# Kernel optimization log

Measured on AMD Instinct MI355X. Metric: run time of the kernel, lower is better.

The kernel has to match this reference:

```python
import jax, jax.numpy as jnp
import numpy as np

D = 8        # input_path_dim
S = 64       # cde_state_dim
H = 128      # vf_hidden_dim
OUT = 8      # output_path_dim
T = 2049     # time samples
B = 32       # batch (vmapped)
WIN = 16     # signature_window_size
NWIN = (T - 1) // WIN   # 128 scan steps
II, JJ = np.triu_indices(D, 1)    # Lyndon words of length 2: pairs i<j (P=28)


def setup_inputs() -> dict:
    key = jax.random.key(0)
    ks = jax.random.split(key, 16)
    g = lambda k, shp, fan: (jax.random.normal(k, shp, dtype=jnp.float32) / np.sqrt(fan)).astype(jnp.float32)
    z = lambda n: jnp.zeros((n,), jnp.float32)
    return {
        "ts": jnp.arange(T, dtype=jnp.float32),
        "x": jax.random.normal(ks[0], (B, T, D), dtype=jnp.float32) * 0.1,
        # initial MLP: d -> H -> H -> S, softplus activations
        "Wi0": g(ks[1], (H, D), D), "bi0": z(H),
        "Wi1": g(ks[2], (H, H), H), "bi1": z(H),
        "Wi2": g(ks[3], (S, H), H), "bi2": z(S),
        # vector-field MLP: S -> H -> H -> D*S, softplus hidden, tanh final
        "Wv0": g(ks[4], (H, S), S), "bv0": z(H),
        "Wv1": g(ks[5], (H, H), H), "bv1": z(H),
        "Wv2": g(ks[6], (D * S, H), H), "bv2": z(D * S),
        # readout: S -> OUT
        "Wr": g(ks[7], (OUT, S), S), "br": z(OUT),
    }


def _logsignatures(x):
    """Depth-2 log-signatures of a piecewise-linear path over windows.
    x: (B, T, D). Returns s1: (B, NWIN, D) increments, s2: (B, NWIN, P) Levy areas
    in the Lyndon basis [e_i, e_j], i<j."""
    delta = x[:, 1:] - x[:, :-1]                      # (B, T-1, D)
    delta = delta[:, : NWIN * WIN].reshape(x.shape[0], NWIN, WIN, D)
    s1 = delta.sum(axis=2)                            # (B, NWIN, D)
    cum = jnp.cumsum(delta, axis=2) - delta           # exclusive prefix sums
    M = jnp.einsum("bnwi,bnwj->bnij", cum, delta)    # (B, NWIN, D, D)
    L = 0.5 * (M - jnp.swapaxes(M, -1, -2))           # antisymmetric Levy area
    s2 = L[..., II, JJ]                               # (B, NWIN, P)
    return s1, s2


def reference(ts, x, Wi0, bi0, Wi1, bi1, Wi2, bi2, Wv0, bv0, Wv1, bv1, Wv2, bv2, Wr, br):
    sp = jax.nn.softplus

    def initial(x0):  # (D,) -> (S,)
        z = sp(Wi0 @ x0 + bi0)
        z = sp(Wi1 @ z + bi1)
        return Wi2 @ z + bi2

    def vf(h):  # (S,) -> (D, S): one vector field per input channel
        z = sp(Wv0 @ h + bv0)
        z = sp(Wv1 @ z + bv1)
        return jnp.tanh(Wv2 @ z + bv2).reshape(D, S)

    s1, s2 = _logsignatures(x)

    def single(x0_s, s1_s, s2_s):
        h0 = initial(x0_s)

        def step(h, sig):
            a, b = sig  # depth-1 (D,), depth-2 Lyndon coeffs (P,)
            V = vf(h)                          # (D, S)
            J = jax.jacfwd(vf)(h)              # (D, S, S) Jacobians dV_i/dh
            JV = jnp.einsum("dab,eb->dea", J, V)   # JV[j,i] = J_j @ V_i
            brack = JV[JJ, II] - JV[II, JJ]        # (P, S): [V_i, V_j], i<j
            hn = h + a @ V + b @ brack             # log-ODE step
            return hn, hn

        _, hist = jax.lax.scan(step, h0, (s1_s, s2_s))
        return jnp.concatenate([h0[None], hist], axis=0)   # (NWIN+1, S)

    hist = jax.vmap(single)(x[:, 0], s1, s2)    # (B, NWIN+1, S)
    return jnp.einsum("bns,os->bno", hist, Wr) + br   # evolving readout, identity act
```

## Files before the change

kernel.cpp:

```cpp
#include <hip/hip_runtime.h>
#include <hip/hip_bf16.h>

#define DD 8
#define SS 64
#define HH 128
#define OUTD 8
#define TT 2049
#define BB 32
#define WINW 16
#define NWIN 128
#define PP 28
#define VSTR 516

typedef __attribute__((ext_vector_type(8))) short short8v;
typedef __attribute__((ext_vector_type(4))) float f32x4;

__device__ __forceinline__ float softplus_f(float x){
    return fmaxf(x, 0.f) + __logf(1.f + __expf(-fabsf(x)));
}
__device__ __forceinline__ float tanh_f(float x){
    float e = __expf(2.f * x);
    return 1.f - 2.f / (e + 1.f);
}
__device__ __forceinline__ void sp_sig(float x, float& sp, float& sg){
    float t = __expf(-fabsf(x));
    float r = 1.f / (1.f + t);
    sg = x > 0.f ? r : 1.f - r;
    sp = fmaxf(x, 0.f) - __logf(r);
}
__device__ __forceinline__ unsigned short f2bf(float f){
    return __builtin_bit_cast(unsigned short, __float2bfloat16(f));
}
__device__ __forceinline__ unsigned pk2(float a, float b){
    unsigned lo = (unsigned)__builtin_bit_cast(unsigned short, __float2bfloat16(a));
    unsigned hi = (unsigned)__builtin_bit_cast(unsigned short, __float2bfloat16(b));
    return lo | (hi << 16);
}

__global__ void sig_kernel(const float* __restrict__ x,
                           float* __restrict__ s1o, float* __restrict__ s2o){
    int w = blockIdx.x * blockDim.x + threadIdx.x;
    if (w >= BB * NWIN) return;
    int b = w >> 7, n = w & (NWIN - 1);
    const float* xp = x + ((size_t)b * TT + (size_t)n * WINW) * DD;
    float prev[DD], cum[DD], s1v[DD], M[DD][DD];
    #pragma unroll
    for (int i = 0; i < DD; ++i){
        cum[i] = 0.f; s1v[i] = 0.f;
        #pragma unroll
        for (int j = 0; j < DD; ++j) M[i][j] = 0.f;
    }
    #pragma unroll
    for (int i = 0; i < DD; ++i) prev[i] = xp[i];
    for (int t = 0; t < WINW; ++t){
        float cur[DD], del[DD];
        #pragma unroll
        for (int i = 0; i < DD; ++i) cur[i] = xp[(t + 1) * DD + i];
        #pragma unroll
        for (int i = 0; i < DD; ++i) del[i] = cur[i] - prev[i];
        #pragma unroll
        for (int i = 0; i < DD; ++i){
            #pragma unroll
            for (int j = 0; j < DD; ++j) M[i][j] += cum[i] * del[j];
        }
        #pragma unroll
        for (int i = 0; i < DD; ++i){ cum[i] += del[i]; s1v[i] += del[i]; prev[i] = cur[i]; }
    }
    #pragma unroll
    for (int i = 0; i < DD; ++i) s1o[(size_t)w * DD + i] = s1v[i];
    int p = 0;
    #pragma unroll
    for (int i = 0; i < DD; ++i){
        #pragma unroll
        for (int j = i + 1; j < DD; ++j){ s2o[(size_t)w * PP + p] = 0.5f * (M[i][j] - M[j][i]); ++p; }
    }
}

#define BPOS(k, nn) ((((k) >> 5) * 64 + (((k) >> 3) & 3) * 16 + (nn)) * 8 + ((k) & 7))

__global__ __launch_bounds__(512, 2) void scan_kernel(
    const float* __restrict__ x,
    const float* __restrict__ Wi0, const float* __restrict__ bi0,
    const float* __restrict__ Wi1, const float* __restrict__ bi1,
    const float* __restrict__ Wi2, const float* __restrict__ bi2,
    const float* __restrict__ Wv0, const float* __restrict__ bv0,
    const float* __restrict__ Wv1, const float* __restrict__ bv1,
    const float* __restrict__ Wv2, const float* __restrict__ bv2,
    const float* __restrict__ Wr,  const float* __restrict__ br,
    const float* __restrict__ s1g, const float* __restrict__ s2g,
    float* __restrict__ out)
{
    const int tid = threadIdx.x;
    const int w   = tid >> 6;
    const int l   = tid & 63;
    const int lg  = l >> 4;
    const int ln  = l & 15;
    const int b0  = blockIdx.x * 4;

    __shared__ __align__(16) short BpH[2 * 64 * 8];
    __shared__ __align__(16) short Bp0[4 * 64 * 8];
    __shared__ __align__(16) short Bp1[4 * 64 * 8];
    __shared__ __align__(16) short Bp7[2][2 * 64 * 8];
    __shared__ __align__(16) short Bp8[2][4 * 64 * 8];
    __shared__ __align__(16) short Bp9[2][4 * 64 * 8];
    __shared__ __align__(16) float s0p[4][HH], s1p[4][HH];
    __shared__ __align__(16) float Vl[4 * VSTR], Rf[4 * VSTR];
    __shared__ __align__(16) float hfb[4][2][SS];
    __shared__ __align__(16) float bv0L[HH], bv1L[HH], bv2L[512];
    __shared__ __align__(16) float WrL[OUTD * SS];
    __shared__ float brL[OUTD];
    __shared__ __align__(16) float sAll[4][NWIN * DD];
    __shared__ __align__(16) float bAll[4][NWIN * PP];
    __shared__ __align__(16) float outC[4][32][OUTD];
    __shared__ __align__(16) float Cexp[4][DD][12];

    short8v a0f[2], a1f[4];
    short8v a2f0[4], a2f1[4], a2f2[4], a2f3[4];
    #pragma unroll
    for (int ks = 0; ks < 2; ++ks){
        const float* p = Wv0 + (size_t)(w * 16 + ln) * SS + ks * 32 + lg * 8;
        short8v f;
        #pragma unroll
        for (int j = 0; j < 8; ++j) f[j] = (short)f2bf(p[j]);
        a0f[ks] = f;
    }
    #pragma unroll
    for (int ks = 0; ks < 4; ++ks){
        const float* p = Wv1 + (size_t)(w * 16 + ln) * HH + ks * 32 + lg * 8;
        short8v f;
        #pragma unroll
        for (int j = 0; j < 8; ++j) f[j] = (short)f2bf(p[j]);
        a1f[ks] = f;
    }
    #pragma unroll
    for (int ks = 0; ks < 4; ++ks){
        const float* p0 = Wv2 + (size_t)(64 * w + 0 * 16 + ln) * HH + ks * 32 + lg * 8;
        const float* p1 = Wv2 + (size_t)(64 * w + 1 * 16 + ln) * HH + ks * 32 + lg * 8;
        const float* p2 = Wv2 + (size_t)(64 * w + 2 * 16 + ln) * HH + ks * 32 + lg * 8;
        const float* p3 = Wv2 + (size_t)(64 * w + 3 * 16 + ln) * HH + ks * 32 + lg * 8;
        short8v f0, f1, f2, f3;
        #pragma unroll
        for (int j = 0; j < 8; ++j){
            f0[j] = (short)f2bf(p0[j]); f1[j] = (short)f2bf(p1[j]);
            f2[j] = (short)f2bf(p2[j]); f3[j] = (short)f2bf(p3[j]);
        }
        a2f0[ks] = f0; a2f1[ks] = f1; a2f2[ks] = f2; a2f3[ks] = f3;
    }
    if (tid < HH){ bv0L[tid] = bv0[tid]; bv1L[tid] = bv1[tid]; }
    bv2L[tid] = bv2[tid];
    WrL[tid]  = Wr[tid];
    if (tid < OUTD) brL[tid] = br[tid];
    {
        float* sF = &sAll[0][0];
        for (int i = tid; i < 4 * NWIN * DD; i += 512){
            int c = i >> 10;
            sF[i] = s1g[(size_t)(b0 + c) * (NWIN * DD) + (i & 1023)];
        }
        float* bF = &bAll[0][0];
        for (int i = tid; i < 4 * NWIN * PP; i += 512){
            int c = i / (NWIN * PP);
            bF[i] = s2g[(size_t)(b0 + c) * (NWIN * PP) + (i - c * (NWIN * PP))];
        }
        for (int i = tid; i < 2 * 64 * 8; i += 512) BpH[i] = 0;
        for (int i = tid; i < 4 * 64 * 8; i += 512){ Bp0[i] = 0; Bp1[i] = 0; }
    }
    __syncthreads();

    {
        int c4 = tid >> 7, r = tid & 127;
        float acc = bi0[r];
        const float* x0 = x + (size_t)(b0 + c4) * TT * DD;
        #pragma unroll
        for (int k = 0; k < DD; ++k) acc += Wi0[r * DD + k] * x0[k];
        s0p[c4][r] = softplus_f(acc);
    }
    if (tid < 256){
        int cc = tid >> 6, dd = (tid >> 3) & 7, ee = tid & 7;
        const float* bco = &bAll[cc][0];
        float cv = 0.f;
        if (ee < dd)      cv =  bco[((ee * (15 - ee)) >> 1) + dd - ee - 1];
        else if (ee > dd) cv = -bco[((dd * (15 - dd)) >> 1) + ee - dd - 1];
        Cexp[cc][dd][ee] = cv;
    }
    __syncthreads();
    {
        int c4 = tid >> 7, r = tid & 127;
        float acc = bi1[r];
        const f32x4* wv = (const f32x4*)(Wi1 + (size_t)r * HH);
        const f32x4* zv = (const f32x4*)&s0p[c4][0];
        #pragma unroll 8
        for (int k = 0; k < 32; ++k){
            f32x4 a = wv[k], z = zv[k];
            acc += a.x * z.x + a.y * z.y + a.z * z.z + a.w * z.w;
        }
        s1p[c4][r] = softplus_f(acc);
    }
    __syncthreads();
    if (tid < 256){
        int c4 = tid >> 6, s = tid & 63;
        float acc = bi2[s];
        const f32x4* wv = (const f32x4*)(Wi2 + (size_t)s * HH);
        const f32x4* zv = (const f32x4*)&s1p[c4][0];
        #pragma unroll 8
        for (int k = 0; k < 32; ++k){
            f32x4 a = wv[k], z = zv[k];
            acc += a.x * z.x + a.y * z.y + a.z * z.z + a.w * z.w;
        }
        hfb[c4][0][s] = acc;
        BpH[BPOS(s, c4)] = (short)f2bf(acc);
    }
    __syncthreads();

    const f32x4 zero4 = {0.f, 0.f, 0.f, 0.f};
    const int rb = w * 16 + lg * 4;

    for (int n = 0; n < NWIN; ++n){
        {
            f32x4 acc = zero4;
            acc = __builtin_amdgcn_mfma_f32_16x16x32_bf16(a0f[0], *(const short8v*)&BpH[(0 * 64 + l) * 8], acc, 0, 0, 0);
            acc = __builtin_amdgcn_mfma_f32_16x16x32_bf16(a0f[1], *(const short8v*)&BpH[(1 * 64 + l) * 8], acc, 0, 0, 0);
            if (ln < 4){
                int c = ln;
                f32x4 bv = *(const f32x4*)&bv0L[rb];
                float z[4], sgv[4];
                #pragma unroll
                for (int r = 0; r < 4; ++r){
                    float zz, gg;
                    sp_sig(acc[r] + bv[r], zz, gg);
                    z[r] = zz; sgv[r] = gg;
                }
                f32x4 sg = {sgv[0], sgv[1], sgv[2], sgv[3]};
                *(f32x4*)&s0p[c][rb] = sg;
                uint2 pk; pk.x = pk2(z[0], z[1]); pk.y = pk2(z[2], z[3]);
                *(uint2*)&Bp0[BPOS(rb, c)] = pk;
            }
        }
        __syncthreads();

        {
            f32x4 acc = zero4;
            #pragma unroll
            for (int ks = 0; ks < 4; ++ks)
                acc = __builtin_amdgcn_mfma_f32_16x16x32_bf16(a1f[ks], *(const short8v*)&Bp0[(ks * 64 + l) * 8], acc, 0, 0, 0);
            if (ln < 4){
                int c = ln;
                f32x4 bv = *(const f32x4*)&bv1L[rb];
                float z[4], sgv[4];
                #pragma unroll
                for (int r = 0; r < 4; ++r){
                    float zz, gg;
                    sp_sig(acc[r] + bv[r], zz, gg);
                    z[r] = zz; sgv[r] = gg;
                }
                f32x4 sg = {sgv[0], sgv[1], sgv[2], sgv[3]};
                *(f32x4*)&s1p[c][rb] = sg;
                uint2 pk; pk.x = pk2(z[0], z[1]); pk.y = pk2(z[2], z[3]);
                #pragma unroll
                for (int cc = 0; cc < 4; ++cc) *(uint2*)&Bp1[BPOS(rb, c * 4 + cc)] = pk;
            }
        }
        __syncthreads();

        {
            short8v bf[4];
            #pragma unroll
            for (int ks = 0; ks < 4; ++ks) bf[ks] = *(const short8v*)&Bp1[(ks * 64 + l) * 8];
            f32x4 acc0 = zero4, acc1 = zero4, acc2 = zero4, acc3 = zero4;
            #pragma unroll
            for (int ks = 0; ks < 4; ++ks){
                acc0 = __builtin_amdgcn_mfma_f32_16x16x32_bf16(a2f0[ks], bf[ks], acc0, 0, 0, 0);
                acc1 = __builtin_amdgcn_mfma_f32_16x16x32_bf16(a2f1[ks], bf[ks], acc1, 0, 0, 0);
                acc2 = __builtin_amdgcn_mfma_f32_16x16x32_bf16(a2f2[ks], bf[ks], acc2, 0, 0, 0);
                acc3 = __builtin_amdgcn_mfma_f32_16x16x32_bf16(a2f3[ks], bf[ks], acc3, 0, 0, 0);
            }
            {
                int c = ln >> 2, t = ln & 3;
                f32x4 av = (t == 0) ? acc0 : (t == 1) ? acc1 : (t == 2) ? acc2 : acc3;
                int r4 = 64 * w + t * 16 + lg * 4;
                f32x4 bv = *(const f32x4*)&bv2L[r4];
                f32x4 vv;
                #pragma unroll
                for (int r = 0; r < 4; ++r) vv[r] = tanh_f(av[r] + bv[r]);
                *(f32x4*)&Vl[c * VSTR + r4] = vv;
            }
        }
        __syncthreads();

        {
            int c = tid >> 7, d = (tid >> 4) & 7, s0v = (tid & 15) * 4;
            f32x4 cm0 = *(const f32x4*)&Cexp[c][d][0];
            f32x4 cm1 = *(const f32x4*)&Cexp[c][d][4];
            f32x4 acc = zero4;
            #pragma unroll
            for (int e = 0; e < 8; ++e){
                float ce = (e < 4) ? cm0[e] : cm1[e - 4];
                f32x4 v4 = *(const f32x4*)&Vl[c * VSTR + e * 64 + s0v];
                acc.x += ce * v4.x; acc.y += ce * v4.y;
                acc.z += ce * v4.z; acc.w += ce * v4.w;
            }
            uint2 pk; pk.x = pk2(acc.x, acc.y); pk.y = pk2(acc.z, acc.w);
            *(uint2*)&Bp7[c >> 1][BPOS(s0v, (c & 1) * 8 + d)] = pk;
        }
        __syncthreads();

        {
            #pragma unroll
            for (int p = 0; p < 2; ++p){
                f32x4 acc = zero4;
                acc = __builtin_amdgcn_mfma_f32_16x16x32_bf16(a0f[0], *(const short8v*)&Bp7[p][(0 * 64 + l) * 8], acc, 0, 0, 0);
                acc = __builtin_amdgcn_mfma_f32_16x16x32_bf16(a0f[1], *(const short8v*)&Bp7[p][(1 * 64 + l) * 8], acc, 0, 0, 0);
                int c = 2 * p + (ln >> 3);
                f32x4 sg = *(const f32x4*)&s0p[c][rb];
                uint2 pk; pk.x = pk2(sg[0] * acc[0], sg[1] * acc[1]);
                pk.y = pk2(sg[2] * acc[2], sg[3] * acc[3]);
                *(uint2*)&Bp8[p][BPOS(rb, ln)] = pk;
            }
        }
        __syncthreads();

        {
            #pragma unroll
            for (int p = 0; p < 2; ++p){
                f32x4 acc = zero4;
                #pragma unroll
                for (int ks = 0; ks < 4; ++ks)
                    acc = __builtin_amdgcn_mfma_f32_16x16x32_bf16(a1f[ks], *(const short8v*)&Bp8[p][(ks * 64 + l) * 8], acc, 0, 0, 0);
                int c = 2 * p + (ln >> 3), d = ln & 7;
                f32x4 sg = *(const f32x4*)&s1p[c][rb];
                uint2 pk; pk.x = pk2(sg[0] * acc[0], sg[1] * acc[1]);
                pk.y = pk2(sg[2] * acc[2], sg[3] * acc[3]);
                *(uint2*)&Bp9[d >> 2][BPOS(rb, (d & 3) * 4 + c)] = pk;
            }
        }
        __syncthreads();

        {
            const int im = w >> 2;
            short8v bf[4];
            #pragma unroll
            for (int ks = 0; ks < 4; ++ks) bf[ks] = *(const short8v*)&Bp9[im][(ks * 64 + l) * 8];
            f32x4 acc0 = zero4, acc1 = zero4, acc2 = zero4, acc3 = zero4;
            #pragma unroll
            for (int ks = 0; ks < 4; ++ks){
                acc0 = __builtin_amdgcn_mfma_f32_16x16x32_bf16(a2f0[ks], bf[ks], acc0, 0, 0, 0);
                acc1 = __builtin_amdgcn_mfma_f32_16x16x32_bf16(a2f1[ks], bf[ks], acc1, 0, 0, 0);
                acc2 = __builtin_amdgcn_mfma_f32_16x16x32_bf16(a2f2[ks], bf[ks], acc2, 0, 0, 0);
                acc3 = __builtin_amdgcn_mfma_f32_16x16x32_bf16(a2f3[ks], bf[ks], acc3, 0, 0, 0);
            }
            if ((ln >> 2) == (w & 3)){
                int c = ln & 3;
                #pragma unroll
                for (int t = 0; t < 4; ++t){
                    f32x4 av = (t == 0) ? acc0 : (t == 1) ? acc1 : (t == 2) ? acc2 : acc3;
                    int r4 = 64 * w + t * 16 + lg * 4;
                    f32x4 vv = *(const f32x4*)&Vl[c * VSTR + r4];
                    f32x4 rr;
                    #pragma unroll
                    for (int r = 0; r < 4; ++r) rr[r] = (1.f - vv[r] * vv[r]) * av[r];
                    *(f32x4*)&Rf[c * VSTR + r4] = rr;
                }
            }
        }
        __syncthreads();

        {
            const int cur = n & 1;
            if (w < 4){
                int c = w, s = l;
                f32x4 a0 = *(const f32x4*)&sAll[c][n * DD];
                f32x4 a1 = *(const f32x4*)&sAll[c][n * DD + 4];
                float hN = hfb[c][cur][s];
                #pragma unroll
                for (int d = 0; d < 4; ++d)
                    hN += a0[d] * Vl[c * VSTR + d * 64 + s] + Rf[c * VSTR + d * 64 + s];
                #pragma unroll
                for (int d = 4; d < 8; ++d)
                    hN += a1[d - 4] * Vl[c * VSTR + d * 64 + s] + Rf[c * VSTR + d * 64 + s];
                hfb[c][cur ^ 1][s] = hN;
                BpH[BPOS(s, c)] = (short)f2bf(hN);
            } else {
                {
                    int idx = (w - 4) * 64 + l;
                    int cc = idx >> 6, dd = (idx >> 3) & 7, ee = idx & 7;
                    int nn = (n + 1 < NWIN) ? n + 1 : NWIN - 1;
                    const float* bco = &bAll[cc][nn * PP];
                    float cv = 0.f;
                    if (ee < dd)      cv =  bco[((ee * (15 - ee)) >> 1) + dd - ee - 1];
                    else if (ee > dd) cv = -bco[((dd * (15 - dd)) >> 1) + ee - dd - 1];
                    Cexp[cc][dd][ee] = cv;
                }
                int c = w - 4;
                int o = l >> 3, qq = l & 7;
                f32x4 w0 = *(const f32x4*)&WrL[o * SS + qq * 8];
                f32x4 w1 = *(const f32x4*)&WrL[o * SS + qq * 8 + 4];
                f32x4 h0 = *(const f32x4*)&hfb[c][cur][qq * 8];
                f32x4 h1 = *(const f32x4*)&hfb[c][cur][qq * 8 + 4];
                float acc = w0.x*h0.x + w0.y*h0.y + w0.z*h0.z + w0.w*h0.w
                          + w1.x*h1.x + w1.y*h1.y + w1.z*h1.z + w1.w*h1.w;
                acc += __shfl_xor(acc, 1); acc += __shfl_xor(acc, 2); acc += __shfl_xor(acc, 4);
                if (qq == 0) outC[c][n & 31][o] = brL[o] + acc;
                if ((n & 31) == 31){
                    size_t base = (size_t)(b0 + c) * (NWIN + 1) * OUTD + (size_t)(n - 31) * OUTD;
                    const f32x4* oc = (const f32x4*)&outC[c][0][0];
                    f32x4 v = oc[l];
                    *(f32x4*)&out[base + l * 4] = v;
                }
            }
        }
        __syncthreads();
    }

    if (w >= 4){
        int c = w - 4;
        int o = l >> 3, qq = l & 7;
        f32x4 w0 = *(const f32x4*)&WrL[o * SS + qq * 8];
        f32x4 w1 = *(const f32x4*)&WrL[o * SS + qq * 8 + 4];
        f32x4 h0 = *(const f32x4*)&hfb[c][0][qq * 8];
        f32x4 h1 = *(const f32x4*)&hfb[c][0][qq * 8 + 4];
        float acc = w0.x*h0.x + w0.y*h0.y + w0.z*h0.z + w0.w*h0.w
                  + w1.x*h1.x + w1.y*h1.y + w1.z*h1.z + w1.w*h1.w;
        acc += __shfl_xor(acc, 1); acc += __shfl_xor(acc, 2); acc += __shfl_xor(acc, 4);
        if (qq == 0)
            out[(size_t)(b0 + c) * (NWIN + 1) * OUTD + (size_t)NWIN * OUTD + o] = brL[o] + acc;
    }
}

extern "C" void kernel_launch(void* const* d_in, const int* in_sizes, int n_in,
                              void* d_out, int out_size, void* d_ws, size_t ws_size,
                              hipStream_t stream){
    const float* x   = (const float*)d_in[1];
    const float* Wi0 = (const float*)d_in[2];
    const float* bi0 = (const float*)d_in[3];
    const float* Wi1 = (const float*)d_in[4];
    const float* bi1 = (const float*)d_in[5];
    const float* Wi2 = (const float*)d_in[6];
    const float* bi2 = (const float*)d_in[7];
    const float* Wv0 = (const float*)d_in[8];
    const float* bv0 = (const float*)d_in[9];
    const float* Wv1 = (const float*)d_in[10];
    const float* bv1 = (const float*)d_in[11];
    const float* Wv2 = (const float*)d_in[12];
    const float* bv2 = (const float*)d_in[13];
    const float* Wr  = (const float*)d_in[14];
    const float* br  = (const float*)d_in[15];
    float* out = (float*)d_out;

    float* s1w = (float*)d_ws;
    float* s2w = s1w + (size_t)BB * NWIN * DD;

    sig_kernel<<<(BB * NWIN + 255) / 256, 256, 0, stream>>>(x, s1w, s2w);
    scan_kernel<<<BB / 4, 512, 0, stream>>>(x, Wi0, bi0, Wi1, bi1, Wi2, bi2,
                                            Wv0, bv0, Wv1, bv1, Wv2, bv2,
                                            Wr, br, s1w, s2w, out);
}
```

Baseline: 520.0 us.

## Double scan block to 1024 threads and split MFMA work across 16 waves

Launches the recurrent scan kernel with 1024 threads (16 waves) instead of 512. Each wave now holds half as many Wv2 output rows, and the two Jacobian-vector passes are split across wave halves instead of looped. MFMA accumulation chains are split into two independent accumulators that are summed, which shortens dependency latency. The Cexp precompute moves to otherwise idle waves. The aim is to cut per-step latency on the serial 128-step recurrence, at the cost of more threads taking part in each block barrier.

```diff
diff --git a/kernel.cpp b/kernel.cpp
--- a/kernel.cpp
+++ b/kernel.cpp
@@ -78,7 +78,8 @@
 
 #define BPOS(k, nn) ((((k) >> 5) * 64 + (((k) >> 3) & 3) * 16 + (nn)) * 8 + ((k) & 7))
 
-__global__ __launch_bounds__(512, 2) void scan_kernel(
+__global__ __attribute__((amdgpu_flat_work_group_size(1024, 1024), amdgpu_waves_per_eu(4)))
+void scan_kernel(
     const float* __restrict__ x,
     const float* __restrict__ Wi0, const float* __restrict__ bi0,
     const float* __restrict__ Wi1, const float* __restrict__ bi1,
@@ -95,6 +96,7 @@
     const int l   = tid & 63;
     const int lg  = l >> 4;
     const int ln  = l & 15;
+    const int wm  = w & 7;
     const int b0  = blockIdx.x * 4;
 
     __shared__ __align__(16) short BpH[2 * 64 * 8];
@@ -115,10 +117,10 @@
     __shared__ __align__(16) float Cexp[4][DD][12];
 
     short8v a0f[2], a1f[4];
-    short8v a2f0[4], a2f1[4], a2f2[4], a2f3[4];
+    short8v a2f0[4], a2f1[4];
     #pragma unroll
     for (int ks = 0; ks < 2; ++ks){
-        const float* p = Wv0 + (size_t)(w * 16 + ln) * SS + ks * 32 + lg * 8;
+        const float* p = Wv0 + (size_t)(wm * 16 + ln) * SS + ks * 32 + lg * 8;
         short8v f;
         #pragma unroll
         for (int j = 0; j < 8; ++j) f[j] = (short)f2bf(p[j]);
@@ -126,7 +128,7 @@
     }
     #pragma unroll
     for (int ks = 0; ks < 4; ++ks){
-        const float* p = Wv1 + (size_t)(w * 16 + ln) * HH + ks * 32 + lg * 8;
+        const float* p = Wv1 + (size_t)(wm * 16 + ln) * HH + ks * 32 + lg * 8;
         short8v f;
         #pragma unroll
         for (int j = 0; j < 8; ++j) f[j] = (short)f2bf(p[j]);
@@ -134,48 +136,44 @@
     }
     #pragma unroll
     for (int ks = 0; ks < 4; ++ks){
-        const float* p0 = Wv2 + (size_t)(64 * w + 0 * 16 + ln) * HH + ks * 32 + lg * 8;
-        const float* p1 = Wv2 + (size_t)(64 * w + 1 * 16 + ln) * HH + ks * 32 + lg * 8;
-        const float* p2 = Wv2 + (size_t)(64 * w + 2 * 16 + ln) * HH + ks * 32 + lg * 8;
-        const float* p3 = Wv2 + (size_t)(64 * w + 3 * 16 + ln) * HH + ks * 32 + lg * 8;
-        short8v f0, f1, f2, f3;
+        const float* p0 = Wv2 + (size_t)(32 * w + 0 * 16 + ln) * HH + ks * 32 + lg * 8;
+        const float* p1 = Wv2 + (size_t)(32 * w + 1 * 16 + ln) * HH + ks * 32 + lg * 8;
+        short8v f0, f1;
         #pragma unroll
         for (int j = 0; j < 8; ++j){
             f0[j] = (short)f2bf(p0[j]); f1[j] = (short)f2bf(p1[j]);
-            f2[j] = (short)f2bf(p2[j]); f3[j] = (short)f2bf(p3[j]);
-        }
-        a2f0[ks] = f0; a2f1[ks] = f1; a2f2[ks] = f2; a2f3[ks] = f3;
+        }
+        a2f0[ks] = f0; a2f1[ks] = f1;
     }
     if (tid < HH){ bv0L[tid] = bv0[tid]; bv1L[tid] = bv1[tid]; }
-    bv2L[tid] = bv2[tid];
-    WrL[tid]  = Wr[tid];
+    if (tid < 512){ bv2L[tid] = bv2[tid]; WrL[tid] = Wr[tid]; }
     if (tid < OUTD) brL[tid] = br[tid];
     {
         float* sF = &sAll[0][0];
-        for (int i = tid; i < 4 * NWIN * DD; i += 512){
+        for (int i = tid; i < 4 * NWIN * DD; i += 1024){
             int c = i >> 10;
             sF[i] = s1g[(size_t)(b0 + c) * (NWIN * DD) + (i & 1023)];
         }
         float* bF = &bAll[0][0];
-        for (int i = tid; i < 4 * NWIN * PP; i += 512){
+        for (int i = tid; i < 4 * NWIN * PP; i += 1024){
             int c = i / (NWIN * PP);
             bF[i] = s2g[(size_t)(b0 + c) * (NWIN * PP) + (i - c * (NWIN * PP))];
         }
-        for (int i = tid; i < 2 * 64 * 8; i += 512) BpH[i] = 0;
-        for (int i = tid; i < 4 * 64 * 8; i += 512){ Bp0[i] = 0; Bp1[i] = 0; }
+        for (int i = tid; i < 2 * 64 * 8; i += 1024) BpH[i] = 0;
+        for (int i = tid; i < 4 * 64 * 8; i += 1024){ Bp0[i] = 0; Bp1[i] = 0; }
     }
     __syncthreads();
 
-    {
+    if (tid < 512){
         int c4 = tid >> 7, r = tid & 127;
         float acc = bi0[r];
         const float* x0 = x + (size_t)(b0 + c4) * TT * DD;
         #pragma unroll
         for (int k = 0; k < DD; ++k) acc += Wi0[r * DD + k] * x0[k];
         s0p[c4][r] = softplus_f(acc);
-    }
-    if (tid < 256){
-        int cc = tid >> 6, dd = (tid >> 3) & 7, ee = tid & 7;
+    } else if (tid < 768){
+        int t2 = tid - 512;
+        int cc = t2 >> 6, dd = (t2 >> 3) & 7, ee = t2 & 7;
         const float* bco = &bAll[cc][0];
         float cv = 0.f;
         if (ee < dd)      cv =  bco[((ee * (15 - ee)) >> 1) + dd - ee - 1];
@@ -183,7 +181,7 @@
         Cexp[cc][dd][ee] = cv;
     }
     __syncthreads();
-    {
+    if (tid < 512){
         int c4 = tid >> 7, r = tid & 127;
         float acc = bi1[r];
         const f32x4* wv = (const f32x4*)(Wi1 + (size_t)r * HH);
@@ -212,13 +210,14 @@
     __syncthreads();
 
     const f32x4 zero4 = {0.f, 0.f, 0.f, 0.f};
-    const int rb = w * 16 + lg * 4;
+    const int rb = wm * 16 + lg * 4;
 
     for (int n = 0; n < NWIN; ++n){
-        {
-            f32x4 acc = zero4;
-            acc = __builtin_amdgcn_mfma_f32_16x16x32_bf16(a0f[0], *(const short8v*)&BpH[(0 * 64 + l) * 8], acc, 0, 0, 0);
-            acc = __builtin_amdgcn_mfma_f32_16x16x32_bf16(a0f[1], *(const short8v*)&BpH[(1 * 64 + l) * 8], acc, 0, 0, 0);
+        if (w < 8){
+            f32x4 accA = zero4, accB = zero4;
+            accA = __builtin_amdgcn_mfma_f32_16x16x32_bf16(a0f[0], *(const short8v*)&BpH[(0 * 64 + l) * 8], accA, 0, 0, 0);
+            accB = __builtin_amdgcn_mfma_f32_16x16x32_bf16(a0f[1], *(const short8v*)&BpH[(1 * 64 + l) * 8], accB, 0, 0, 0);
+            f32x4 acc = accA + accB;
             if (ln < 4){
                 int c = ln;
                 f32x4 bv = *(const f32x4*)&bv0L[rb];
@@ -237,11 +236,13 @@
         }
         __syncthreads();
 
-        {
-            f32x4 acc = zero4;
-            #pragma unroll
-            for (int ks = 0; ks < 4; ++ks)
-                acc = __builtin_amdgcn_mfma_f32_16x16x32_bf16(a1f[ks], *(const short8v*)&Bp0[(ks * 64 + l) * 8], acc, 0, 0, 0);
+        if (w < 8){
+            f32x4 accA = zero4, accB = zero4;
+            accA = __builtin_amdgcn_mfma_f32_16x16x32_bf16(a1f[0], *(const short8v*)&Bp0[(0 * 64 + l) * 8], accA, 0, 0, 0);
+            accA = __builtin_amdgcn_mfma_f32_16x16x32_bf16(a1f[1], *(const short8v*)&Bp0[(1 * 64 + l) * 8], accA, 0, 0, 0);
+            accB = __builtin_amdgcn_mfma_f32_16x16x32_bf16(a1f[2], *(const short8v*)&Bp0[(2 * 64 + l) * 8], accB, 0, 0, 0);
+            accB = __builtin_amdgcn_mfma_f32_16x16x32_bf16(a1f[3], *(const short8v*)&Bp0[(3 * 64 + l) * 8], accB, 0, 0, 0);
+            f32x4 acc = accA + accB;
             if (ln < 4){
                 int c = ln;
                 f32x4 bv = *(const f32x4*)&bv1L[rb];
@@ -265,18 +266,20 @@
             short8v bf[4];
             #pragma unroll
             for (int ks = 0; ks < 4; ++ks) bf[ks] = *(const short8v*)&Bp1[(ks * 64 + l) * 8];
-            f32x4 acc0 = zero4, acc1 = zero4, acc2 = zero4, acc3 = zero4;
-            #pragma unroll
-            for (int ks = 0; ks < 4; ++ks){
-                acc0 = __builtin_amdgcn_mfma_f32_16x16x32_bf16(a2f0[ks], bf[ks], acc0, 0, 0, 0);
-                acc1 = __builtin_amdgcn_mfma_f32_16x16x32_bf16(a2f1[ks], bf[ks], acc1, 0, 0, 0);
-                acc2 = __builtin_amdgcn_mfma_f32_16x16x32_bf16(a2f2[ks], bf[ks], acc2, 0, 0, 0);
-                acc3 = __builtin_amdgcn_mfma_f32_16x16x32_bf16(a2f3[ks], bf[ks], acc3, 0, 0, 0);
-            }
-            {
+            f32x4 a0A = zero4, a0B = zero4, a1A = zero4, a1B = zero4;
+            a0A = __builtin_amdgcn_mfma_f32_16x16x32_bf16(a2f0[0], bf[0], a0A, 0, 0, 0);
+            a0A = __builtin_amdgcn_mfma_f32_16x16x32_bf16(a2f0[1], bf[1], a0A, 0, 0, 0);
+            a0B = __builtin_amdgcn_mfma_f32_16x16x32_bf16(a2f0[2], bf[2], a0B, 0, 0, 0);
+            a0B = __builtin_amdgcn_mfma_f32_16x16x32_bf16(a2f0[3], bf[3], a0B, 0, 0, 0);
+            a1A = __builtin_amdgcn_mfma_f32_16x16x32_bf16(a2f1[0], bf[0], a1A, 0, 0, 0);
+            a1A = __builtin_amdgcn_mfma_f32_16x16x32_bf16(a2f1[1], bf[1], a1A, 0, 0, 0);
+            a1B = __builtin_amdgcn_mfma_f32_16x16x32_bf16(a2f1[2], bf[2], a1B, 0, 0, 0);
+            a1B = __builtin_amdgcn_mfma_f32_16x16x32_bf16(a2f1[3], bf[3], a1B, 0, 0, 0);
+            f32x4 acc0 = a0A + a0B, acc1 = a1A + a1B;
+            if ((ln & 3) < 2){
                 int c = ln >> 2, t = ln & 3;
-                f32x4 av = (t == 0) ? acc0 : (t == 1) ? acc1 : (t == 2) ? acc2 : acc3;
-                int r4 = 64 * w + t * 16 + lg * 4;
+                f32x4 av = t ? acc1 : acc0;
+                int r4 = 32 * w + t * 16 + lg * 4;
                 f32x4 bv = *(const f32x4*)&bv2L[r4];
                 f32x4 vv;
                 #pragma unroll
@@ -286,7 +289,7 @@
         }
         __syncthreads();
 
-        {
+        if (tid < 512){
             int c = tid >> 7, d = (tid >> 4) & 7, s0v = (tid & 15) * 4;
             f32x4 cm0 = *(const f32x4*)&Cexp[c][d][0];
             f32x4 cm1 = *(const f32x4*)&Cexp[c][d][4];
@@ -304,55 +307,56 @@
         __syncthreads();
 
         {
-            #pragma unroll
-            for (int p = 0; p < 2; ++p){
-                f32x4 acc = zero4;
-                acc = __builtin_amdgcn_mfma_f32_16x16x32_bf16(a0f[0], *(const short8v*)&Bp7[p][(0 * 64 + l) * 8], acc, 0, 0, 0);
-                acc = __builtin_amdgcn_mfma_f32_16x16x32_bf16(a0f[1], *(const short8v*)&Bp7[p][(1 * 64 + l) * 8], acc, 0, 0, 0);
-                int c = 2 * p + (ln >> 3);
-                f32x4 sg = *(const f32x4*)&s0p[c][rb];
-                uint2 pk; pk.x = pk2(sg[0] * acc[0], sg[1] * acc[1]);
-                pk.y = pk2(sg[2] * acc[2], sg[3] * acc[3]);
-                *(uint2*)&Bp8[p][BPOS(rb, ln)] = pk;
-            }
+            const int p = w >> 3;
+            f32x4 accA = zero4, accB = zero4;
+            accA = __builtin_amdgcn_mfma_f32_16x16x32_bf16(a0f[0], *(const short8v*)&Bp7[p][(0 * 64 + l) * 8], accA, 0, 0, 0);
+            accB = __builtin_amdgcn_mfma_f32_16x16x32_bf16(a0f[1], *(const short8v*)&Bp7[p][(1 * 64 + l) * 8], accB, 0, 0, 0);
+            f32x4 acc = accA + accB;
+            int c = 2 * p + (ln >> 3);
+            f32x4 sg = *(const f32x4*)&s0p[c][rb];
+            uint2 pk; pk.x = pk2(sg[0] * acc[0], sg[1] * acc[1]);
+            pk.y = pk2(sg[2] * acc[2], sg[3] * acc[3]);
+            *(uint2*)&Bp8[p][BPOS(rb, ln)] = pk;
         }
         __syncthreads();
 
         {
-            #pragma unroll
-            for (int p = 0; p < 2; ++p){
-                f32x4 acc = zero4;
-                #pragma unroll
-                for (int ks = 0; ks < 4; ++ks)
-                    acc = __builtin_amdgcn_mfma_f32_16x16x32_bf16(a1f[ks], *(const short8v*)&Bp8[p][(ks * 64 + l) * 8], acc, 0, 0, 0);
-                int c = 2 * p + (ln >> 3), d = ln & 7;
-                f32x4 sg = *(const f32x4*)&s1p[c][rb];
-                uint2 pk; pk.x = pk2(sg[0] * acc[0], sg[1] * acc[1]);
-                pk.y = pk2(sg[2] * acc[2], sg[3] * acc[3]);
-                *(uint2*)&Bp9[d >> 2][BPOS(rb, (d & 3) * 4 + c)] = pk;
-            }
+            const int p = w >> 3;
+            f32x4 accA = zero4, accB = zero4;
+            accA = __builtin_amdgcn_mfma_f32_16x16x32_bf16(a1f[0], *(const short8v*)&Bp8[p][(0 * 64 + l) * 8], accA, 0, 0, 0);
+            accA = __builtin_amdgcn_mfma_f32_16x16x32_bf16(a1f[1], *(const short8v*)&Bp8[p][(1 * 64 + l) * 8], accA, 0, 0, 0);
+            accB = __builtin_amdgcn_mfma_f32_16x16x32_bf16(a1f[2], *(const short8v*)&Bp8[p][(2 * 64 + l) * 8], accB, 0, 0, 0);
+            accB = __builtin_amdgcn_mfma_f32_16x16x32_bf16(a1f[3], *(const short8v*)&Bp8[p][(3 * 64 + l) * 8], accB, 0, 0, 0);
+            f32x4 acc = accA + accB;
+            int c = 2 * p + (ln >> 3), d = ln & 7;
+            f32x4 sg = *(const f32x4*)&s1p[c][rb];
+            uint2 pk; pk.x = pk2(sg[0] * acc[0], sg[1] * acc[1]);
+            pk.y = pk2(sg[2] * acc[2], sg[3] * acc[3]);
+            *(uint2*)&Bp9[d >> 2][BPOS(rb, (d & 3) * 4 + c)] = pk;
         }
         __syncthreads();
 
         {
-            const int im = w >> 2;
+            const int im = w >> 3;
             short8v bf[4];
             #pragma unroll
             for (int ks = 0; ks < 4; ++ks) bf[ks] = *(const short8v*)&Bp9[im][(ks * 64 + l) * 8];
-            f32x4 acc0 = zero4, acc1 = zero4, acc2 = zero4, acc3 = zero4;
-            #pragma unroll
-            for (int ks = 0; ks < 4; ++ks){
-                acc0 = __builtin_amdgcn_mfma_f32_16x16x32_bf16(a2f0[ks], bf[ks], acc0, 0, 0, 0);
-                acc1 = __builtin_amdgcn_mfma_f32_16x16x32_bf16(a2f1[ks], bf[ks], acc1, 0, 0, 0);
-                acc2 = __builtin_amdgcn_mfma_f32_16x16x32_bf16(a2f2[ks], bf[ks], acc2, 0, 0, 0);
-                acc3 = __builtin_amdgcn_mfma_f32_16x16x32_bf16(a2f3[ks], bf[ks], acc3, 0, 0, 0);
-            }
-            if ((ln >> 2) == (w & 3)){
+            f32x4 a0A = zero4, a0B = zero4, a1A = zero4, a1B = zero4;
+            a0A = __builtin_amdgcn_mfma_f32_16x16x32_bf16(a2f0[0], bf[0], a0A, 0, 0, 0);
+            a0A = __builtin_amdgcn_mfma_f32_16x16x32_bf16(a2f0[1], bf[1], a0A, 0, 0, 0);
+            a0B = __builtin_amdgcn_mfma_f32_16x16x32_bf16(a2f0[2], bf[2], a0B, 0, 0, 0);
+            a0B = __builtin_amdgcn_mfma_f32_16x16x32_bf16(a2f0[3], bf[3], a0B, 0, 0, 0);
+            a1A = __builtin_amdgcn_mfma_f32_16x16x32_bf16(a2f1[0], bf[0], a1A, 0, 0, 0);
+            a1A = __builtin_amdgcn_mfma_f32_16x16x32_bf16(a2f1[1], bf[1], a1A, 0, 0, 0);
+            a1B = __builtin_amdgcn_mfma_f32_16x16x32_bf16(a2f1[2], bf[2], a1B, 0, 0, 0);
+            a1B = __builtin_amdgcn_mfma_f32_16x16x32_bf16(a2f1[3], bf[3], a1B, 0, 0, 0);
+            f32x4 acc0 = a0A + a0B, acc1 = a1A + a1B;
+            if ((ln >> 2) == ((w >> 1) & 3)){
                 int c = ln & 3;
                 #pragma unroll
-                for (int t = 0; t < 4; ++t){
-                    f32x4 av = (t == 0) ? acc0 : (t == 1) ? acc1 : (t == 2) ? acc2 : acc3;
-                    int r4 = 64 * w + t * 16 + lg * 4;
+                for (int t = 0; t < 2; ++t){
+                    f32x4 av = t ? acc1 : acc0;
+                    int r4 = 32 * w + t * 16 + lg * 4;
                     f32x4 vv = *(const f32x4*)&Vl[c * VSTR + r4];
                     f32x4 rr;
                     #pragma unroll
@@ -378,17 +382,7 @@
                     hN += a1[d - 4] * Vl[c * VSTR + d * 64 + s] + Rf[c * VSTR + d * 64 + s];
                 hfb[c][cur ^ 1][s] = hN;
                 BpH[BPOS(s, c)] = (short)f2bf(hN);
-            } else {
-                {
-                    int idx = (w - 4) * 64 + l;
-                    int cc = idx >> 6, dd = (idx >> 3) & 7, ee = idx & 7;
-                    int nn = (n + 1 < NWIN) ? n + 1 : NWIN - 1;
-                    const float* bco = &bAll[cc][nn * PP];
-                    float cv = 0.f;
-                    if (ee < dd)      cv =  bco[((ee * (15 - ee)) >> 1) + dd - ee - 1];
-                    else if (ee > dd) cv = -bco[((dd * (15 - dd)) >> 1) + ee - dd - 1];
-                    Cexp[cc][dd][ee] = cv;
-                }
+            } else if (w < 8){
                 int c = w - 4;
                 int o = l >> 3, qq = l & 7;
                 f32x4 w0 = *(const f32x4*)&WrL[o * SS + qq * 8];
@@ -405,12 +399,21 @@
                     f32x4 v = oc[l];
                     *(f32x4*)&out[base + l * 4] = v;
                 }
-            }
-        }
-        __syncthreads();
-    }
-
-    if (w >= 4){
+            } else if (w < 12){
+                int idx = (w - 8) * 64 + l;
+                int cc = idx >> 6, dd = (idx >> 3) & 7, ee = idx & 7;
+                int nn = (n + 1 < NWIN) ? n + 1 : NWIN - 1;
+                const float* bco = &bAll[cc][nn * PP];
+                float cv = 0.f;
+                if (ee < dd)      cv =  bco[((ee * (15 - ee)) >> 1) + dd - ee - 1];
+                else if (ee > dd) cv = -bco[((dd * (15 - dd)) >> 1) + ee - dd - 1];
+                Cexp[cc][dd][ee] = cv;
+            }
+        }
+        __syncthreads();
+    }
+
+    if (w >= 4 && w < 8){
         int c = w - 4;
         int o = l >> 3, qq = l & 7;
         f32x4 w0 = *(const f32x4*)&WrL[o * SS + qq * 8];
@@ -449,7 +452,7 @@
     float* s2w = s1w + (size_t)BB * NWIN * DD;
 
     sig_kernel<<<(BB * NWIN + 255) / 256, 256, 0, stream>>>(x, s1w, s2w);
-    scan_kernel<<<BB / 4, 512, 0, stream>>>(x, Wi0, bi0, Wi1, bi1, Wi2, bi2,
-                                            Wv0, bv0, Wv1, bv1, Wv2, bv2,
-                                            Wr, br, s1w, s2w, out);
-}
+    scan_kernel<<<BB / 4, 1024, 0, stream>>>(x, Wi0, bi0, Wi1, bi1, Wi2, bi2,
+                                             Wv0, bv0, Wv1, bv1, Wv2, bv2,
+                                             Wr, br, s1w, s2w, out);
+}
```

New measurement: 584.7 us. 12.4% more time.
